# Kernel tuning notes

Measured on AMD Instinct MI355X. Metric: run time of the kernel, lower is better.

The kernel has to match this reference:

```python
import jax, jax.numpy as jnp
import numpy as np

VOXEL_SIZE = 0.04
M = 32768            # voxels surviving from previous level
V = 9                # views per fragment
C = 24               # image feature channels at finest scale
H, W = 120, 160      # fine feature map size (640x480 images /4)
C_PRE = 50           # channels[1] + tsdf + occ from previous level
UP_OFFSETS = np.array([[0,0,0,0],[0,1,0,0],[0,0,1,0],[0,0,0,1],
                       [0,1,1,0],[0,1,0,1],[0,0,1,1],[0,1,1,1]], dtype=np.int32)


def setup_inputs():
    key = jax.random.key(0)
    ks = jax.random.split(key, 10)
    pre_feat = jax.random.normal(ks[0], (M, C_PRE), jnp.float32)
    xyz = jax.random.randint(ks[1], (M, 3), 0, 94).astype(jnp.int32)
    pre_coords = jnp.concatenate([jnp.zeros((M, 1), jnp.int32), xyz], axis=1)
    feats = jax.random.normal(ks[2], (V, 1, C, H, W), jnp.float32)
    # plausible pinhole KRcam = K @ [R|t], identity rotation, jittered translation
    fx = fy = 100.0
    cx, cy = (W - 1) / 2.0, (H - 1) / 2.0
    K = np.array([[fx, 0, cx, 0], [0, fy, cy, 0], [0, 0, 1, 0], [0, 0, 0, 1]], np.float32)
    t = np.asarray(jax.random.uniform(ks[3], (V, 3), minval=-0.2, maxval=0.2))
    RT = np.tile(np.eye(4, dtype=np.float32), (V, 1, 1))
    RT[:, :3, 3] = t
    KRcam = jnp.asarray(np.einsum('ij,vjk->vik', K, RT).astype(np.float32))[:, None]  # (V,1,4,4)
    vol_origin = jnp.array([[-1.9, -1.9, 0.5]], jnp.float32)
    w2ac = jnp.asarray(np.eye(4, dtype=np.float32)[None]) + 0.01 * jax.random.normal(ks[4], (1, 4, 4), jnp.float32)
    W_sp = jax.random.normal(ks[5], (C + 1 + C_PRE, 24), jnp.float32) * 0.1
    b_sp = jnp.zeros((24,), jnp.float32)
    W_t = jax.random.normal(ks[6], (24, 1), jnp.float32) * 0.1
    b_t = jnp.zeros((1,), jnp.float32)
    W_o = jax.random.normal(ks[7], (24, 1), jnp.float32) * 0.1
    b_o = jnp.zeros((1,), jnp.float32)
    return dict(pre_feat=pre_feat, pre_coords=pre_coords, feats=feats, KRcam=KRcam,
                vol_origin=vol_origin, world_to_aligned_camera=w2ac,
                W_sp=W_sp, b_sp=b_sp, W_t=W_t, b_t=b_t, W_o=W_o, b_o=b_o)


def upsample(pre_feat, pre_coords, interval):
    # 1 -> 8 octree coordinate upsample (NeuConHead.upsample)
    off = jnp.asarray(UP_OFFSETS) * interval          # batch col stays 0
    up_coords = (pre_coords[:, None, :] + off[None]).reshape(-1, 4)
    up_feat = jnp.broadcast_to(pre_feat[:, None, :], (pre_feat.shape[0], 8, pre_feat.shape[1])).reshape(-1, pre_feat.shape[1])
    return up_feat, up_coords


def back_project(coords_xyz, origin, voxel_size, feats, KRcam):
    # coords_xyz: (N,3) int voxel coords; feats: (V,C,H,W); KRcam: (V,4,4)
    n = coords_xyz.shape[0]
    world = coords_xyz.astype(jnp.float32) * voxel_size + origin          # (N,3)
    homog = jnp.concatenate([world, jnp.ones((n, 1), jnp.float32)], 1)    # (N,4)
    im_p = jnp.einsum('vij,nj->vin', KRcam, homog)                        # (V,4,N)
    im_x, im_y, im_z = im_p[:, 0], im_p[:, 1], im_p[:, 2]
    safe_z = jnp.where(jnp.abs(im_z) > 1e-9, im_z, 1e-9)
    px = im_x / safe_z
    py = im_y / safe_z
    mask = (px >= 0) & (px <= W - 1) & (py >= 0) & (py <= H - 1) & (im_z > 0)  # (V,N)

    def sample_view(img, x, y, m):
        # bilinear grid_sample, align_corners=True, zero padding; img (C,H,W)
        x0 = jnp.floor(x); y0 = jnp.floor(y)
        wx = x - x0; wy = y - y0
        def gather(xi, yi):
            ok = (xi >= 0) & (xi < W) & (yi >= 0) & (yi < H)
            v = img[:, jnp.clip(yi, 0, H - 1).astype(jnp.int32), jnp.clip(xi, 0, W - 1).astype(jnp.int32)]
            return v * ok  # (C,N)
        top = gather(x0, y0) * (1 - wx) + gather(x0 + 1, y0) * wx
        bot = gather(x0, y0 + 1) * (1 - wx) + gather(x0 + 1, y0 + 1) * wx
        return jnp.where(m, top * (1 - wy) + bot * wy, 0.0)  # (C,N)

    fsamp = jax.vmap(sample_view)(feats, px, py, mask)        # (V,C,N)
    zed = jnp.where(mask, im_z, 0.0)                          # (V,N)
    count = mask.sum(0).astype(jnp.float32)                   # (N,)
    denom = jnp.maximum(count, 1.0)
    features = fsamp.sum(0) / denom                           # (C,N)
    z = zed.sum(0) / denom                                    # (N,)
    pos = z > 0
    npos = jnp.maximum(pos.sum(), 1).astype(jnp.float32)
    zmean = jnp.where(pos, z, 0.0).sum() / npos
    znorm = jnp.sqrt(jnp.where(pos, (z - zmean) ** 2, 0.0).sum()) + 1e-5  # torch.norm
    zn = jnp.where(pos, (z - zmean) / znorm, 0.0)
    volume = jnp.concatenate([features.T, zn[:, None]], axis=1)  # (N, C+1)
    return volume, count


def reference(pre_feat, feats, KRcam, vol_origin, world_to_aligned_camera,
              W_sp, b_sp, W_t, b_t, W_o, b_o, pre_coords):
    up_feat, up_coords = upsample(pre_feat, pre_coords, 1)
    volume, count = back_project(up_coords[:, 1:], vol_origin[0], VOXEL_SIZE,
                                 feats[:, 0], KRcam[:, 0])
    feat = jnp.concatenate([volume, up_feat], axis=1)          # (N, 75)
    # r_coords: world -> aligned camera frame (bs=1)
    world = up_coords[:, 1:].astype(jnp.float32) * VOXEL_SIZE + vol_origin[0]
    homog = jnp.concatenate([world, jnp.ones_like(world[:, :1])], axis=1)
    cam = homog @ world_to_aligned_camera[0, :3, :].T          # (N,3)
    r_coords = jnp.concatenate([cam, up_coords[:, :1].astype(jnp.float32)], axis=1)
    h = jax.nn.relu(feat @ W_sp + b_sp)                        # SPVCNN stand-in head
    tsdf = h @ W_t + b_t
    occ = h @ W_o + b_o
    out = jnp.concatenate([tsdf, occ], axis=1)                 # (N,2)
    return out, count, r_coords
```

## Files before the change

kernel.cpp:

```cpp
#include <hip/hip_runtime.h>
#include <hip/hip_fp16.h>

#define Mpts 32768
#define Vv 9
#define Cc 24
#define Hh 120
#define Ww 160
#define Npts (Mpts * 8)
#define PIX (Hh * Ww)
#define VOXEL 0.04f

#define NB_TF   ((Vv * PIX) / 256)
#define NB_GEMM (Mpts / 256)
#define NB_Z    (Npts / 256)

#define OFF_RED   0
#define OFF_TF16  32768
#define OFF_TF8   (OFF_TF16 + Vv * PIX * 16)
#define OFF_PREH  (OFF_TF8 + Vv * PIX * 8)

typedef __attribute__((ext_vector_type(2))) float f32x2;
typedef __attribute__((ext_vector_type(4))) float f32x4;
typedef __attribute__((ext_vector_type(4))) int i32x4;

__device__ __forceinline__ uint4 ld_u4_a8(const void* p) {
  struct __attribute__((packed, aligned(8))) A8 { uint4 v; };
  return ((const A8*)p)->v;
}

__device__ __forceinline__ unsigned pack4fp8(float a, float b, float c,
                                             float d) {
  int u = __builtin_amdgcn_cvt_pk_fp8_f32(a, b, 0, false);
  u = __builtin_amdgcn_cvt_pk_fp8_f32(c, d, u, true);
  return (unsigned)u;
}

__global__ __launch_bounds__(256) void prep_kernel(
    const float* __restrict__ feats, const float* __restrict__ pre_feat,
    const float* __restrict__ W_sp, const float* __restrict__ b_sp,
    const int* __restrict__ pre_coords, const float* __restrict__ KRcam,
    const float* __restrict__ vol_origin, const float* __restrict__ w2ac,
    uint4* __restrict__ tf16, uint2* __restrict__ tf8,
    float* __restrict__ pre_h, double* __restrict__ red,
    float* __restrict__ out) {
  __shared__ float Wl[50 * Cc];
  __shared__ float bl[Cc];
  __shared__ float KRs[Vv * 12];
  __shared__ float origs[3];
  __shared__ float redl[3][4];
  int blk = blockIdx.x;

  if (blk < NB_TF) {
    int gp = blk * 256 + threadIdx.x;
    int v = gp / PIX;
    int p = gp - v * PIX;
    const float* src = feats + (size_t)v * (Cc * PIX) + p;
    float t[Cc];
#pragma unroll
    for (int c = 0; c < Cc; c++)
      t[c] = __builtin_nontemporal_load(src + (size_t)c * PIX);
    uint4 u;
    u.x = pack4fp8(t[0], t[1], t[2], t[3]);
    u.y = pack4fp8(t[4], t[5], t[6], t[7]);
    u.z = pack4fp8(t[8], t[9], t[10], t[11]);
    u.w = pack4fp8(t[12], t[13], t[14], t[15]);
    tf16[gp] = u;
    uint2 u2;
    u2.x = pack4fp8(t[16], t[17], t[18], t[19]);
    u2.y = pack4fp8(t[20], t[21], t[22], t[23]);
    tf8[gp] = u2;
  } else if (blk < NB_TF + NB_GEMM) {
    int mb = blk - NB_TF;
    for (int i = threadIdx.x; i < 50 * Cc; i += 256) Wl[i] = W_sp[25 * Cc + i];
    if (threadIdx.x < Cc) bl[threadIdx.x] = b_sp[threadIdx.x];
    __syncthreads();
    int m = mb * 256 + threadIdx.x;
    float acc[Cc];
#pragma unroll
    for (int j = 0; j < Cc; j++) acc[j] = bl[j];
    const f32x2* pf = (const f32x2*)(pre_feat + (size_t)m * 50);
#pragma unroll 5
    for (int k = 0; k < 25; k++) {
      f32x2 x = __builtin_nontemporal_load(pf + k);
#pragma unroll
      for (int j = 0; j < Cc; j++)
        acc[j] += x.x * Wl[(2 * k) * Cc + j] + x.y * Wl[(2 * k + 1) * Cc + j];
    }
    f32x4* o4 = (f32x4*)(pre_h + (size_t)m * Cc);
#pragma unroll
    for (int t = 0; t < 6; t++) {
      f32x4 v4 = {acc[4 * t], acc[4 * t + 1], acc[4 * t + 2], acc[4 * t + 3]};
      o4[t] = v4;
    }
  } else {
    int zblk = blk - (NB_TF + NB_GEMM);
    for (int i = threadIdx.x; i < Vv * 12; i += 256) {
      int v = i / 12, r = i - v * 12;
      KRs[i] = KRcam[v * 16 + r];
    }
    if (threadIdx.x < 3) origs[threadIdx.x] = vol_origin[threadIdx.x];
    __syncthreads();
    int n = zblk * 256 + threadIdx.x;
    int m = n >> 3, o = n & 7;
    i32x4 pc = __builtin_nontemporal_load((const i32x4*)pre_coords + m);
    int cx = pc.y + ((0xB2 >> o) & 1);
    int cy = pc.z + ((0xD4 >> o) & 1);
    int cz = pc.w + ((0xE8 >> o) & 1);
    float wx0 = (float)cx * VOXEL + origs[0];
    float wy0 = (float)cy * VOXEL + origs[1];
    float wz0 = (float)cz * VOXEL + origs[2];

    {
      float camx = w2ac[0] * wx0 + w2ac[1] * wy0 + w2ac[2] * wz0 + w2ac[3];
      float camy = w2ac[4] * wx0 + w2ac[5] * wy0 + w2ac[6] * wz0 + w2ac[7];
      float camz = w2ac[8] * wx0 + w2ac[9] * wy0 + w2ac[10] * wz0 + w2ac[11];
      f32x4 rc = {camx, camy, camz, (float)pc.x};
      __builtin_nontemporal_store(rc, (f32x4*)(out + 3 * (size_t)Npts) + n);
    }

    float zsum = 0.f;
    int cnt = 0;
    for (int v = 0; v < Vv; v++) {
      const float* kr = &KRs[v * 12];
      float ix = kr[0] * wx0 + kr[1] * wy0 + kr[2] * wz0 + kr[3];
      float iy = kr[4] * wx0 + kr[5] * wy0 + kr[6] * wz0 + kr[7];
      float iz = kr[8] * wx0 + kr[9] * wy0 + kr[10] * wz0 + kr[11];
      float sz = (fabsf(iz) > 1e-9f) ? iz : 1e-9f;
      float px = ix / sz;
      float py = iy / sz;
      bool msk = (px >= 0.f) && (px <= (float)(Ww - 1)) && (py >= 0.f) &&
                 (py <= (float)(Hh - 1)) && (iz > 0.f);
      if (msk) {
        zsum += iz;
        cnt++;
      }
    }
    float denom = fmaxf((float)cnt, 1.f);
    float z = zsum / denom;
    float rz = (z > 0.f) ? z : 0.f;
    float rz2 = rz * rz;
    float rcn = (z > 0.f) ? 1.f : 0.f;
#pragma unroll
    for (int off = 32; off > 0; off >>= 1) {
      rz += __shfl_down(rz, off);
      rz2 += __shfl_down(rz2, off);
      rcn += __shfl_down(rcn, off);
    }
    int wid = threadIdx.x >> 6, lid = threadIdx.x & 63;
    if (lid == 0) {
      redl[0][wid] = rz;
      redl[1][wid] = rz2;
      redl[2][wid] = rcn;
    }
    __syncthreads();
    if (threadIdx.x == 0) {
      float a = 0.f, b = 0.f, c = 0.f;
#pragma unroll
      for (int w = 0; w < 4; w++) {
        a += redl[0][w];
        b += redl[1][w];
        c += redl[2][w];
      }
      double* r3 = red + (size_t)zblk * 3;
      r3[0] = (double)a;
      r3[1] = (double)b;
      r3[2] = (double)c;
    }
  }
}

__device__ __forceinline__ void acc16(uint4 A, float w, float* acc) {
#pragma unroll
  for (int t = 0; t < 4; t++) {
    unsigned u = ((const unsigned*)&A)[t];
    f32x2 f0 = __builtin_amdgcn_cvt_pk_f32_fp8((int)u, false);
    f32x2 f1 = __builtin_amdgcn_cvt_pk_f32_fp8((int)u, true);
    acc[4 * t + 0] += w * f0.x;
    acc[4 * t + 1] += w * f0.y;
    acc[4 * t + 2] += w * f1.x;
    acc[4 * t + 3] += w * f1.y;
  }
}
__device__ __forceinline__ void acc8v(unsigned ux, unsigned uy, float w,
                                      float* acc) {
  f32x2 f0 = __builtin_amdgcn_cvt_pk_f32_fp8((int)ux, false);
  f32x2 f1 = __builtin_amdgcn_cvt_pk_f32_fp8((int)ux, true);
  f32x2 f2 = __builtin_amdgcn_cvt_pk_f32_fp8((int)uy, false);
  f32x2 f3 = __builtin_amdgcn_cvt_pk_f32_fp8((int)uy, true);
  acc[0] += w * f0.x;
  acc[1] += w * f0.y;
  acc[2] += w * f1.x;
  acc[3] += w * f1.y;
  acc[4] += w * f2.x;
  acc[5] += w * f2.y;
  acc[6] += w * f3.x;
  acc[7] += w * f3.y;
}

__global__ __launch_bounds__(256, 4) void main_kernel(
    const int* __restrict__ pre_coords, const uint4* __restrict__ tf16,
    const unsigned char* __restrict__ tf8, const float* __restrict__ KRcam,
    const float* __restrict__ vol_origin, const float* __restrict__ W_sp,
    const float* __restrict__ W_t, const float* __restrict__ b_t,
    const float* __restrict__ W_o, const float* __restrict__ b_o,
    const float* __restrict__ pre_h, float* __restrict__ out,
    const double* __restrict__ red) {
  __shared__ float KR[Vv * 12];
  __shared__ float orig[3];
  __shared__ double dredl[3][4];
  __shared__ float s_zmean, s_izn;
  for (int i = threadIdx.x; i < Vv * 12; i += 256) {
    int v = i / 12, r = i - v * 12;
    KR[i] = KRcam[v * 16 + r];
  }
  if (threadIdx.x < 3) orig[threadIdx.x] = vol_origin[threadIdx.x];

  {
    double a = 0.0, b = 0.0, c = 0.0;
    for (int s = threadIdx.x; s < NB_Z; s += 256) {
      const double* r3 = red + (size_t)s * 3;
      a += r3[0];
      b += r3[1];
      c += r3[2];
    }
#pragma unroll
    for (int off = 32; off > 0; off >>= 1) {
      a += __shfl_down(a, off);
      b += __shfl_down(b, off);
      c += __shfl_down(c, off);
    }
    int wid = threadIdx.x >> 6, lid = threadIdx.x & 63;
    if (lid == 0) {
      dredl[0][wid] = a;
      dredl[1][wid] = b;
      dredl[2][wid] = c;
    }
    __syncthreads();
    if (threadIdx.x == 0) {
      double A = 0.0, B = 0.0, C = 0.0;
#pragma unroll
      for (int w = 0; w < 4; w++) {
        A += dredl[0][w];
        B += dredl[1][w];
        C += dredl[2][w];
      }
      double npos = (C > 0.0) ? C : 1.0;
      double zmean = A / npos;
      double var = B - 2.0 * zmean * A + C * zmean * zmean;
      if (var < 0.0) var = 0.0;
      double znorm = sqrt(var) + 1e-5;
      s_zmean = (float)zmean;
      s_izn = (float)(1.0 / znorm);
    }
  }
  __syncthreads();

  int n = blockIdx.x * 256 + threadIdx.x;
  int m = n >> 3, o = n & 7;
  i32x4 pc = __builtin_nontemporal_load((const i32x4*)pre_coords + m);
  int cx = pc.y + ((0xB2 >> o) & 1);
  int cy = pc.z + ((0xD4 >> o) & 1);
  int cz = pc.w + ((0xE8 >> o) & 1);
  float wx0 = (float)cx * VOXEL + orig[0];
  float wy0 = (float)cy * VOXEL + orig[1];
  float wz0 = (float)cz * VOXEL + orig[2];

  float acc[Cc];
#pragma unroll
  for (int c = 0; c < Cc; c++) acc[c] = 0.f;
  float zsum = 0.f;
  int cnt = 0;

  for (int v = 0; v < Vv; v++) {
    const float* kr = &KR[v * 12];
    float ix = kr[0] * wx0 + kr[1] * wy0 + kr[2] * wz0 + kr[3];
    float iy = kr[4] * wx0 + kr[5] * wy0 + kr[6] * wz0 + kr[7];
    float iz = kr[8] * wx0 + kr[9] * wy0 + kr[10] * wz0 + kr[11];
    float sz = (fabsf(iz) > 1e-9f) ? iz : 1e-9f;
    float px = ix / sz;
    float py = iy / sz;
    bool msk = (px >= 0.f) && (px <= (float)(Ww - 1)) && (py >= 0.f) &&
               (py <= (float)(Hh - 1)) && (iz > 0.f);
    if (msk) {
      int x0 = (int)floorf(px), y0 = (int)floorf(py);
      int xs = min(x0, Ww - 2), ys = min(y0, Hh - 2);
      float wx = px - (float)xs, wy = py - (float)ys;
      float w00 = (1.f - wx) * (1.f - wy);
      float w10 = wx * (1.f - wy);
      float w01 = (1.f - wx) * wy;
      float w11 = wx * wy;
      size_t pp = (size_t)(v * PIX + ys * Ww + xs);
      const uint4* h16 = tf16 + pp;
      uint4 A = h16[0], B = h16[1];
      uint4 C = h16[Ww], D = h16[Ww + 1];
      const unsigned char* t8 = tf8 + pp * 8;
      uint4 Tab = ld_u4_a8(t8);
      uint4 Tcd = ld_u4_a8(t8 + Ww * 8);
      acc16(A, w00, &acc[0]);
      acc16(B, w10, &acc[0]);
      acc16(C, w01, &acc[0]);
      acc16(D, w11, &acc[0]);
      acc8v(Tab.x, Tab.y, w00, &acc[16]);
      acc8v(Tab.z, Tab.w, w10, &acc[16]);
      acc8v(Tcd.x, Tcd.y, w01, &acc[16]);
      acc8v(Tcd.z, Tcd.w, w11, &acc[16]);
      zsum += iz;
      cnt++;
    }
  }

  float denom = fmaxf((float)cnt, 1.f);
  float invd = 1.f / denom;
  float z = zsum * invd;

  float h[Cc];
  {
    const f32x4* ph4 = (const f32x4*)(pre_h + (size_t)m * Cc);
#pragma unroll
    for (int t = 0; t < 6; t++) {
      f32x4 v4 = ph4[t];
      h[4 * t + 0] = v4.x;
      h[4 * t + 1] = v4.y;
      h[4 * t + 2] = v4.z;
      h[4 * t + 3] = v4.w;
    }
  }
#pragma unroll
  for (int c = 0; c < Cc; c++) {
    float f = acc[c] * invd;
#pragma unroll
    for (int j = 0; j < Cc; j++) h[j] += f * W_sp[c * Cc + j];
  }

  float zn = (z > 0.f) ? (z - s_zmean) * s_izn : 0.f;
  float tsdf = b_t[0], occ = b_o[0];
#pragma unroll
  for (int j = 0; j < Cc; j++) {
    float hj = fmaxf(h[j] + zn * W_sp[24 * Cc + j], 0.f);
    tsdf += hj * W_t[j];
    occ += hj * W_o[j];
  }
  f32x2 o2 = {tsdf, occ};
  __builtin_nontemporal_store(o2, (f32x2*)out + n);
  __builtin_nontemporal_store((float)cnt, out + 2 * (size_t)Npts + n);
}

extern "C" void kernel_launch(void* const* d_in, const int* in_sizes, int n_in,
                              void* d_out, int out_size, void* d_ws,
                              size_t ws_size, hipStream_t stream) {
  const float* pre_feat = (const float*)d_in[0];
  const int* pre_coords = (const int*)d_in[1];
  const float* feats = (const float*)d_in[2];
  const float* KRcam = (const float*)d_in[3];
  const float* vol_origin = (const float*)d_in[4];
  const float* w2ac = (const float*)d_in[5];
  const float* W_sp = (const float*)d_in[6];
  const float* b_sp = (const float*)d_in[7];
  const float* W_t = (const float*)d_in[8];
  const float* b_t = (const float*)d_in[9];
  const float* W_o = (const float*)d_in[10];
  const float* b_o = (const float*)d_in[11];

  float* out = (float*)d_out;
  char* ws = (char*)d_ws;
  double* red = (double*)(ws + OFF_RED);
  uint4* tf16 = (uint4*)(ws + OFF_TF16);
  uint2* tf8 = (uint2*)(ws + OFF_TF8);
  float* pre_h = (float*)(ws + OFF_PREH);

  prep_kernel<<<NB_TF + NB_GEMM + NB_Z, 256, 0, stream>>>(
      feats, pre_feat, W_sp, b_sp, pre_coords, KRcam, vol_origin, w2ac, tf16,
      tf8, pre_h, red, out);
  main_kernel<<<NB_Z, 256, 0, stream>>>(
      pre_coords, tf16, (const unsigned char*)tf8, KRcam, vol_origin, W_sp,
      W_t, b_t, W_o, b_o, pre_h, out, red);
}
```

Measured before the change: 129.3 us.

## Split bilinear gather across two lanes per voxel and combine with shuffle

Each voxel is now handled by two adjacent threads, one per bilinear row (top or bottom), which halves the per-thread gather loads and accumulation. The partial 24-channel accumulators are combined with a lane-xor shuffle, and only the even lane runs the small MLP and writes outputs. The grid doubles and launch bounds rise to 8 blocks per CU to allow more memory-level parallelism. In exchange the projection math is duplicated, half the lanes sit idle during the MLP, and the block prologue (including the reduction) runs twice as often.

```diff
diff --git a/kernel.cpp b/kernel.cpp
--- a/kernel.cpp
+++ b/kernel.cpp
@@ -13,6 +13,7 @@
 #define NB_TF   ((Vv * PIX) / 256)
 #define NB_GEMM (Mpts / 256)
 #define NB_Z    (Npts / 256)
+#define NB_MAIN ((2 * Npts) / 256)
 
 #define OFF_RED   0
 #define OFF_TF16  32768
@@ -197,7 +198,7 @@
   acc[7] += w * f3.y;
 }
 
-__global__ __launch_bounds__(256, 4) void main_kernel(
+__global__ __launch_bounds__(256, 8) void main_kernel(
     const int* __restrict__ pre_coords, const uint4* __restrict__ tf16,
     const unsigned char* __restrict__ tf8, const float* __restrict__ KRcam,
     const float* __restrict__ vol_origin, const float* __restrict__ W_sp,
@@ -255,9 +256,11 @@
   }
   __syncthreads();
 
-  int n = blockIdx.x * 256 + threadIdx.x;
+  int g = blockIdx.x * 256 + threadIdx.x;
+  int n = g >> 1;
+  int q = g & 1;
   int m = n >> 3, o = n & 7;
-  i32x4 pc = __builtin_nontemporal_load((const i32x4*)pre_coords + m);
+  i32x4 pc = ((const i32x4*)pre_coords)[m];
   int cx = pc.y + ((0xB2 >> o) & 1);
   int cy = pc.z + ((0xD4 >> o) & 1);
   int cz = pc.w + ((0xE8 >> o) & 1);
@@ -285,64 +288,60 @@
       int x0 = (int)floorf(px), y0 = (int)floorf(py);
       int xs = min(x0, Ww - 2), ys = min(y0, Hh - 2);
       float wx = px - (float)xs, wy = py - (float)ys;
-      float w00 = (1.f - wx) * (1.f - wy);
-      float w10 = wx * (1.f - wy);
-      float w01 = (1.f - wx) * wy;
-      float w11 = wx * wy;
-      size_t pp = (size_t)(v * PIX + ys * Ww + xs);
-      const uint4* h16 = tf16 + pp;
-      uint4 A = h16[0], B = h16[1];
-      uint4 C = h16[Ww], D = h16[Ww + 1];
-      const unsigned char* t8 = tf8 + pp * 8;
-      uint4 Tab = ld_u4_a8(t8);
-      uint4 Tcd = ld_u4_a8(t8 + Ww * 8);
-      acc16(A, w00, &acc[0]);
-      acc16(B, w10, &acc[0]);
-      acc16(C, w01, &acc[0]);
-      acc16(D, w11, &acc[0]);
-      acc8v(Tab.x, Tab.y, w00, &acc[16]);
-      acc8v(Tab.z, Tab.w, w10, &acc[16]);
-      acc8v(Tcd.x, Tcd.y, w01, &acc[16]);
-      acc8v(Tcd.z, Tcd.w, w11, &acc[16]);
+      float fy = q ? wy : (1.f - wy);
+      float wA = (1.f - wx) * fy;
+      float wB = wx * fy;
+      size_t pp = (size_t)(v * PIX + (ys + q) * Ww + xs);
+      uint4 A = tf16[pp], B = tf16[pp + 1];
+      uint4 T = ld_u4_a8(tf8 + pp * 8);
+      acc16(A, wA, &acc[0]);
+      acc16(B, wB, &acc[0]);
+      acc8v(T.x, T.y, wA, &acc[16]);
+      acc8v(T.z, T.w, wB, &acc[16]);
       zsum += iz;
       cnt++;
     }
   }
 
-  float denom = fmaxf((float)cnt, 1.f);
-  float invd = 1.f / denom;
-  float z = zsum * invd;
-
-  float h[Cc];
-  {
-    const f32x4* ph4 = (const f32x4*)(pre_h + (size_t)m * Cc);
-#pragma unroll
-    for (int t = 0; t < 6; t++) {
-      f32x4 v4 = ph4[t];
-      h[4 * t + 0] = v4.x;
-      h[4 * t + 1] = v4.y;
-      h[4 * t + 2] = v4.z;
-      h[4 * t + 3] = v4.w;
-    }
-  }
-#pragma unroll
-  for (int c = 0; c < Cc; c++) {
-    float f = acc[c] * invd;
-#pragma unroll
-    for (int j = 0; j < Cc; j++) h[j] += f * W_sp[c * Cc + j];
-  }
-
-  float zn = (z > 0.f) ? (z - s_zmean) * s_izn : 0.f;
-  float tsdf = b_t[0], occ = b_o[0];
-#pragma unroll
-  for (int j = 0; j < Cc; j++) {
-    float hj = fmaxf(h[j] + zn * W_sp[24 * Cc + j], 0.f);
-    tsdf += hj * W_t[j];
-    occ += hj * W_o[j];
-  }
-  f32x2 o2 = {tsdf, occ};
-  __builtin_nontemporal_store(o2, (f32x2*)out + n);
-  __builtin_nontemporal_store((float)cnt, out + 2 * (size_t)Npts + n);
+#pragma unroll
+  for (int c = 0; c < Cc; c++) acc[c] += __shfl_xor(acc[c], 1);
+
+  if (q == 0) {
+    float denom = fmaxf((float)cnt, 1.f);
+    float invd = 1.f / denom;
+    float z = zsum * invd;
+
+    float h[Cc];
+    {
+      const f32x4* ph4 = (const f32x4*)(pre_h + (size_t)m * Cc);
+#pragma unroll
+      for (int t = 0; t < 6; t++) {
+        f32x4 v4 = ph4[t];
+        h[4 * t + 0] = v4.x;
+        h[4 * t + 1] = v4.y;
+        h[4 * t + 2] = v4.z;
+        h[4 * t + 3] = v4.w;
+      }
+    }
+#pragma unroll
+    for (int c = 0; c < Cc; c++) {
+      float f = acc[c] * invd;
+#pragma unroll
+      for (int j = 0; j < Cc; j++) h[j] += f * W_sp[c * Cc + j];
+    }
+
+    float zn = (z > 0.f) ? (z - s_zmean) * s_izn : 0.f;
+    float tsdf = b_t[0], occ = b_o[0];
+#pragma unroll
+    for (int j = 0; j < Cc; j++) {
+      float hj = fmaxf(h[j] + zn * W_sp[24 * Cc + j], 0.f);
+      tsdf += hj * W_t[j];
+      occ += hj * W_o[j];
+    }
+    f32x2 o2 = {tsdf, occ};
+    __builtin_nontemporal_store(o2, (f32x2*)out + n);
+    __builtin_nontemporal_store((float)cnt, out + 2 * (size_t)Npts + n);
+  }
 }
 
 extern "C" void kernel_launch(void* const* d_in, const int* in_sizes, int n_in,
@@ -371,7 +370,7 @@
   prep_kernel<<<NB_TF + NB_GEMM + NB_Z, 256, 0, stream>>>(
       feats, pre_feat, W_sp, b_sp, pre_coords, KRcam, vol_origin, w2ac, tf16,
       tf8, pre_h, red, out);
-  main_kernel<<<NB_Z, 256, 0, stream>>>(
+  main_kernel<<<NB_MAIN, 256, 0, stream>>>(
       pre_coords, tf16, (const unsigned char*)tf8, KRcam, vol_origin, W_sp,
       W_t, b_t, W_o, b_o, pre_h, out, red);
 }
```

New measurement: 158.0 us. +22.2%, slower.
